# Kernel optimization log

Measured on AMD Instinct MI355X. Metric: run time of the kernel, lower is better.

Reference implementation:

```python
import jax, jax.numpy as jnp
import numpy as np

B, S, DIM = 2, 2048, 2048
NH, NKV = 16, 8
HD = DIM // NH  # 128
ROPE_THETA = 10000.0


def setup_inputs() -> dict:
    key = jax.random.key(0)
    ks = jax.random.split(key, 7)
    std = DIM ** -0.5
    x = jax.random.normal(ks[0], (B, S, DIM), jnp.float32)
    wq = jax.random.normal(ks[1], (NH * HD, DIM), jnp.float32) * std
    wk = jax.random.normal(ks[2], (NKV * HD, DIM), jnp.float32) * std
    wv = jax.random.normal(ks[3], (NKV * HD, DIM), jnp.float32) * std
    wo = jax.random.normal(ks[4], (DIM, NH * HD), jnp.float32) * std
    inv_freq = 1.0 / (ROPE_THETA ** (jnp.arange(0, HD, 2, dtype=jnp.float32) / HD))
    ang = jnp.arange(S, dtype=jnp.float32)[:, None] * inv_freq[None, :]  # [S, HD//2]
    freqs_cos = jnp.cos(ang)
    freqs_sin = jnp.sin(ang)
    # diffusion-style random per-batch token mask: t ~ U[0,1) per batch row
    t = jax.random.uniform(ks[5], (B, 1))
    mask = jax.random.uniform(ks[6], (B, S)) < t  # True = masked key
    mask = mask.at[:, 0].set(False)  # first token never masked
    return dict(x=x, wq=wq, wk=wk, wv=wv, wo=wo,
                freqs_cos=freqs_cos, freqs_sin=freqs_sin, mask=mask)


def _rope(x, cos, sin):
    # x: [b, s, h, d]; pairs (x[2i], x[2i+1]) rotated by angle[s, i]
    xr, xi = x[..., 0::2], x[..., 1::2]
    c = cos[None, :, None, :]
    s = sin[None, :, None, :]
    out = jnp.stack([xr * c - xi * s, xr * s + xi * c], axis=-1)
    return out.reshape(x.shape)


def reference(x, wq, wk, wv, wo, freqs_cos, freqs_sin, mask):
    b, s, _ = x.shape
    xq = jnp.einsum('bsd,ed->bse', x, wq).reshape(b, s, NH, HD)
    xk = jnp.einsum('bsd,ed->bse', x, wk).reshape(b, s, NKV, HD)
    xv = jnp.einsum('bsd,ed->bse', x, wv).reshape(b, s, NKV, HD)
    xq = _rope(xq, freqs_cos, freqs_sin)
    xk = _rope(xk, freqs_cos, freqs_sin)
    n_rep = NH // NKV
    xk = jnp.repeat(xk, n_rep, axis=2)  # repeat_kv (GQA)
    xv = jnp.repeat(xv, n_rep, axis=2)
    q = xq.transpose(0, 2, 1, 3)  # [b, h, s, d]
    k = xk.transpose(0, 2, 1, 3)
    v = xv.transpose(0, 2, 1, 3)
    scale = 1.0 / np.sqrt(HD).astype(np.float32)
    scores = jnp.einsum('bhqd,bhkd->bhqk', q, k) * scale  # [b, h, s, s]
    scores = jnp.where(mask[:, None, None, :], -jnp.inf, scores)
    probs = jax.nn.softmax(scores, axis=-1)
    out = jnp.einsum('bhqk,bhkd->bhqd', probs, v)
    out = out.transpose(0, 2, 1, 3).reshape(b, s, NH * HD)
    return jnp.einsum('bse,de->bsd', out, wo)
```

## Files before the change

kernel.cpp:

```cpp
#include <hip/hip_runtime.h>
#include <hip/hip_bf16.h>
#include <cstdint>
#include <cstddef>

#define S_LEN   2048
#define NHQ     16
#define NKV_H   8
#define HD_DIM  128
#define DMODEL  2048
#define BATCH   2
#define KVD     (NKV_H * HD_DIM)

typedef float f32x4  __attribute__((ext_vector_type(4)));
typedef __bf16 bf16x8 __attribute__((ext_vector_type(8)));

__device__ __forceinline__ void gload_lds16(const __bf16* g, __bf16* l) {
    __builtin_amdgcn_global_load_lds(
        (const __attribute__((address_space(1))) void*)g,
        (__attribute__((address_space(3))) void*)l, 16, 0, 0);
}

__global__ void sniff_x_kernel(const unsigned* __restrict__ x,
                               int* __restrict__ flag) {
    __shared__ int cnt;
    if (threadIdx.x == 0) cnt = 0;
    __syncthreads();
    int c = 0;
    for (int j = threadIdx.x; j < 1024; j += 256) {
        unsigned hw = x[j] & 0xFFFFu;
        unsigned e  = (hw >> 7) & 0xFF;
        if (hw == 0u || (e >= 118 && e <= 132)) c++;
    }
    atomicAdd(&cnt, c);
    __syncthreads();
    if (threadIdx.x == 0) *flag = (cnt > 512) ? 1 : 0;
}

__global__ void sniff_fc_kernel(const unsigned* __restrict__ fc,
                                int* __restrict__ flag) {
    if (threadIdx.x == 0) *flag = (fc[0] == 0x3F803F80u) ? 1 : 0;
}

__global__ void mask_norm_kernel(const unsigned char* __restrict__ mraw,
                                 unsigned char* __restrict__ mout, int n) {
    __shared__ int f_bf16, f_f32, f_u8;
    if (threadIdx.x == 0) { f_bf16 = 0; f_f32 = 0; f_u8 = 0; }
    __syncthreads();
    const unsigned* dw = (const unsigned*)mraw;
    int ndw = n / 4;
    for (int j = threadIdx.x; j < ndw; j += blockDim.x) {
        unsigned v = dw[j];
        if (v == 0x00003F80u || v == 0x3F803F80u) f_bf16 = 1;
        else if (v == 0x3F800000u) f_f32 = 1;
        else if (v & 0xFFFFFFFEu) f_u8 = 1;
    }
    __syncthreads();
    int layout;
    if (f_bf16) layout = 3;
    else if (f_f32) layout = 2;
    else if (f_u8) layout = 0;
    else layout = 1;
    for (int i = threadIdx.x; i < n; i += blockDim.x) {
        unsigned v;
        if (layout == 0)      v = mraw[i];
        else if (layout == 3) v = ((const unsigned short*)mraw)[i];
        else                  v = ((const unsigned*)mraw)[i];
        mout[i] = v ? 1u : 0u;
    }
}

__global__ __launch_bounds__(256)
void conv_bf16_kernel(const void* __restrict__ src, __bf16* __restrict__ dst,
                      int n8, const int* __restrict__ dflag) {
    int i = blockIdx.x * blockDim.x + threadIdx.x;
    if (i >= n8) return;
    size_t off = (size_t)i * 8;
    if (*dflag) {
        *reinterpret_cast<uint4*>(dst + off) =
            *reinterpret_cast<const uint4*>((const __bf16*)src + off);
    } else {
        const float* f = (const float*)src + off;
        float4 a = *reinterpret_cast<const float4*>(f);
        float4 b = *reinterpret_cast<const float4*>(f + 4);
        bf16x8 v;
        v[0] = (__bf16)a.x; v[1] = (__bf16)a.y; v[2] = (__bf16)a.z; v[3] = (__bf16)a.w;
        v[4] = (__bf16)b.x; v[5] = (__bf16)b.y; v[6] = (__bf16)b.z; v[7] = (__bf16)b.w;
        *reinterpret_cast<bf16x8*>(dst + off) = v;
    }
}

template <bool OUT_BF16>
__global__ __launch_bounds__(256)
void gemm_bt_async(const __bf16* __restrict__ A, const __bf16* __restrict__ Bw,
                   void* __restrict__ Cv, int M, int N, int K) {
    __shared__ __align__(16) __bf16 As[128 * 64];
    __shared__ __align__(16) __bf16 Bs[128 * 64];

    const int t    = threadIdx.x;
    const int w    = t >> 6;
    const int lane = t & 63;
    const int quad = lane >> 4;
    const int l16  = lane & 15;
    const int wm   = (w >> 1) * 64;
    const int wn   = (w & 1) * 64;
    const int m0   = blockIdx.x * 128;
    const int n0   = blockIdx.y * 128;
    const int rl   = lane >> 3;
    const int gl   = lane & 7;
    const int swA  = (quad) ;

    f32x4 acc[4][4];
#pragma unroll
    for (int i = 0; i < 4; ++i)
#pragma unroll
        for (int j = 0; j < 4; ++j) acc[i][j] = (f32x4){0.f, 0.f, 0.f, 0.f};

    for (int k0 = 0; k0 < K; k0 += 64) {
        __syncthreads();
#pragma unroll
        for (int p = 0; p < 4; ++p) {
            const int rowb = w * 32 + p * 8;
            const int r    = rowb + rl;
            const int gA   = gl ^ rl;
            gload_lds16(A  + (size_t)(m0 + r) * K + k0 + gA * 8, &As[rowb * 64]);
            gload_lds16(Bw + (size_t)(n0 + r) * K + k0 + gA * 8, &Bs[rowb * 64]);
        }
        __syncthreads();
#pragma unroll
        for (int ks = 0; ks < 2; ++ks) {
            const int G = ks * 4 + quad;
            const int gsw = (G ^ (l16 & 7)) * 8;
            bf16x8 af[4], bf[4];
#pragma unroll
            for (int i = 0; i < 4; ++i)
                af[i] = *reinterpret_cast<const bf16x8*>(
                    &As[(wm + i * 16 + l16) * 64 + gsw]);
#pragma unroll
            for (int j = 0; j < 4; ++j)
                bf[j] = *reinterpret_cast<const bf16x8*>(
                    &Bs[(wn + j * 16 + l16) * 64 + gsw]);
#pragma unroll
            for (int i = 0; i < 4; ++i)
#pragma unroll
                for (int j = 0; j < 4; ++j)
                    acc[i][j] = __builtin_amdgcn_mfma_f32_16x16x32_bf16(
                        af[i], bf[j], acc[i][j], 0, 0, 0);
        }
    }
    (void)swA;
#pragma unroll
    for (int i = 0; i < 4; ++i)
#pragma unroll
        for (int r = 0; r < 4; ++r) {
            size_t m = (size_t)(m0 + wm + i * 16 + quad * 4 + r);
#pragma unroll
            for (int j = 0; j < 4; ++j) {
                int n = n0 + wn + j * 16 + l16;
                if constexpr (OUT_BF16)
                    ((__hip_bfloat16*)Cv)[m * N + n] = __float2bfloat16(acc[i][j][r]);
                else
                    ((float*)Cv)[m * N + n] = acc[i][j][r];
            }
        }
}

__global__ void rope_kernel(__hip_bfloat16* __restrict__ xqk,
                            const void* __restrict__ cosv,
                            const void* __restrict__ sinv,
                            const int* __restrict__ dflag_fc,
                            int nheads, int npairs) {
    int idx = blockIdx.x * blockDim.x + threadIdx.x;
    if (idx >= npairs) return;
    int i  = idx & 63;
    int h  = (idx >> 6) % nheads;
    int bs = idx / (64 * nheads);
    int s  = bs & (S_LEN - 1);
    float c, sn;
    if (*dflag_fc) {
        c  = __bfloat162float(((const __hip_bfloat16*)cosv)[s * 64 + i]);
        sn = __bfloat162float(((const __hip_bfloat16*)sinv)[s * 64 + i]);
    } else {
        c  = ((const float*)cosv)[s * 64 + i];
        sn = ((const float*)sinv)[s * 64 + i];
    }
    unsigned* p = (unsigned*)(xqk + (size_t)bs * (nheads * HD_DIM) + h * HD_DIM) + i;
    unsigned u = *p;
    float xr = __uint_as_float(u << 16);
    float xi = __uint_as_float(u & 0xFFFF0000u);
    float o0 = xr * c - xi * sn;
    float o1 = xr * sn + xi * c;
    union { __hip_bfloat16 h2[2]; unsigned u32; } out;
    out.h2[0] = __float2bfloat16(o0);
    out.h2[1] = __float2bfloat16(o1);
    *p = out.u32;
}

__global__ __launch_bounds__(256)
void transpose_v_kernel(const __hip_bfloat16* __restrict__ xv,
                        __hip_bfloat16* __restrict__ vt) {
    __shared__ unsigned short T[32][36];
    const int t  = threadIdx.x;
    const int s0 = blockIdx.x * 32;
    const int d0 = blockIdx.y * 32;
    const int z  = blockIdx.z;
    const int b  = z >> 3;
    const int kv = z & 7;
    {
        int sr = t >> 3, dc = (t & 7) * 4;
        const unsigned short* p = (const unsigned short*)xv
            + (size_t)(b * S_LEN + s0 + sr) * KVD + kv * 128 + d0 + dc;
        uint2 v = *reinterpret_cast<const uint2*>(p);
        T[sr][dc + 0] = (unsigned short)(v.x & 0xFFFFu);
        T[sr][dc + 1] = (unsigned short)(v.x >> 16);
        T[sr][dc + 2] = (unsigned short)(v.y & 0xFFFFu);
        T[sr][dc + 3] = (unsigned short)(v.y >> 16);
    }
    __syncthreads();
    {
        int dr = t >> 3, sc = (t & 7) * 4;
        unsigned w0 = (unsigned)T[sc + 0][dr] | ((unsigned)T[sc + 1][dr] << 16);
        unsigned w1 = (unsigned)T[sc + 2][dr] | ((unsigned)T[sc + 3][dr] << 16);
        unsigned short* q = (unsigned short*)vt
            + ((size_t)z * 128 + d0 + dr) * S_LEN + s0 + sc;
        uint2 v; v.x = w0; v.y = w1;
        *reinterpret_cast<uint2*>(q) = v;
    }
}

__global__ __launch_bounds__(256)
void attn_mfma_kernel(const __hip_bfloat16* xq,
                      const __hip_bfloat16* __restrict__ xk,
                      const __hip_bfloat16* __restrict__ vt_g,
                      const unsigned char* __restrict__ msk,
                      __hip_bfloat16* att) {
    __shared__ __bf16 Qs[64][136];
    __shared__ __bf16 Ks[64][136];
    __shared__ __bf16 Vt[128][72];
    __shared__ __bf16 Ps[4][16][72];

    const int t    = threadIdx.x;
    const int w    = t >> 6;
    const int lane = t & 63;
    const int quad = lane >> 4;
    const int l16  = lane & 15;

    const int bid = blockIdx.x;
    const int qt  = bid & 31;
    const int h   = (bid >> 5) & (NHQ - 1);
    const int b   = bid >> 9;
    const int kvh = h >> 1;
    const int q0  = qt * 64;

#pragma unroll
    for (int i = 0; i < 4; ++i) {
        int p = t + i * 256;
        int r = p >> 4, c = p & 15;
        *reinterpret_cast<uint4*>(&Qs[r][c * 8]) =
            *reinterpret_cast<const uint4*>((const unsigned short*)xq
                + (size_t)(b * S_LEN + q0 + r) * DMODEL + h * 128 + c * 8);
    }

    float m_r[4], l_r[4];
    f32x4 o[8];
#pragma unroll
    for (int r = 0; r < 4; ++r) { m_r[r] = -INFINITY; l_r[r] = 0.f; }
#pragma unroll
    for (int d0 = 0; d0 < 8; ++d0) o[d0] = (f32x4){0.f, 0.f, 0.f, 0.f};

    const float scale = 0.08838834764831845f;

    for (int k0 = 0; k0 < S_LEN; k0 += 64) {
        __syncthreads();
#pragma unroll
        for (int i = 0; i < 4; ++i) {
            int p = t + i * 256;
            int r = p >> 4, c = p & 15;
            *reinterpret_cast<uint4*>(&Ks[r][c * 8]) =
                *reinterpret_cast<const uint4*>((const unsigned short*)xk
                    + (size_t)(b * S_LEN + k0 + r) * KVD + kvh * 128 + c * 8);
        }
#pragma unroll
        for (int i = 0; i < 4; ++i) {
            int p = t + i * 256;
            int d = p >> 3, c = p & 7;
            *reinterpret_cast<uint4*>(&Vt[d][c * 8]) =
                *reinterpret_cast<const uint4*>((const unsigned short*)vt_g
                    + ((size_t)(b * NKV_H + kvh) * 128 + d) * S_LEN + k0 + c * 8);
        }
        int mk[4];
#pragma unroll
        for (int n0 = 0; n0 < 4; ++n0)
            mk[n0] = msk[b * S_LEN + k0 + n0 * 16 + l16];
        __syncthreads();

        f32x4 sc4[4];
#pragma unroll
        for (int n0 = 0; n0 < 4; ++n0) sc4[n0] = (f32x4){0.f, 0.f, 0.f, 0.f};
#pragma unroll
        for (int ks = 0; ks < 4; ++ks) {
            int khd = ks * 32 + quad * 8;
            bf16x8 af = *reinterpret_cast<const bf16x8*>(&Qs[w * 16 + l16][khd]);
#pragma unroll
            for (int n0 = 0; n0 < 4; ++n0) {
                bf16x8 bf = *reinterpret_cast<const bf16x8*>(&Ks[n0 * 16 + l16][khd]);
                sc4[n0] = __builtin_amdgcn_mfma_f32_16x16x32_bf16(af, bf, sc4[n0], 0, 0, 0);
            }
        }

#pragma unroll
        for (int n0 = 0; n0 < 4; ++n0)
#pragma unroll
            for (int r = 0; r < 4; ++r) {
                float v = sc4[n0][r] * scale;
                sc4[n0][r] = mk[n0] ? -INFINITY : v;
            }
        float alpha[4];
#pragma unroll
        for (int r = 0; r < 4; ++r) {
            float rmax = fmaxf(fmaxf(sc4[0][r], sc4[1][r]), fmaxf(sc4[2][r], sc4[3][r]));
#pragma unroll
            for (int m = 1; m < 16; m <<= 1)
                rmax = fmaxf(rmax, __shfl_xor(rmax, m, 64));
            float mn = fmaxf(m_r[r], rmax);
            alpha[r] = __expf(m_r[r] - mn);
            m_r[r] = mn;
            float rs = 0.f;
#pragma unroll
            for (int n0 = 0; n0 < 4; ++n0) {
                float p = __expf(sc4[n0][r] - mn);
                sc4[n0][r] = p;
                rs += p;
            }
#pragma unroll
            for (int m = 1; m < 16; m <<= 1)
                rs += __shfl_xor(rs, m, 64);
            l_r[r] = l_r[r] * alpha[r] + rs;
        }
#pragma unroll
        for (int d0 = 0; d0 < 8; ++d0)
#pragma unroll
            for (int r = 0; r < 4; ++r) o[d0][r] *= alpha[r];

#pragma unroll
        for (int n0 = 0; n0 < 4; ++n0)
#pragma unroll
            for (int r = 0; r < 4; ++r)
                Ps[w][quad * 4 + r][n0 * 16 + l16] = (__bf16)sc4[n0][r];

#pragma unroll
        for (int kk = 0; kk < 64; kk += 32) {
            bf16x8 af = *reinterpret_cast<const bf16x8*>(&Ps[w][l16][kk + quad * 8]);
#pragma unroll
            for (int d0 = 0; d0 < 8; ++d0) {
                bf16x8 bf = *reinterpret_cast<const bf16x8*>(&Vt[d0 * 16 + l16][kk + quad * 8]);
                o[d0] = __builtin_amdgcn_mfma_f32_16x16x32_bf16(af, bf, o[d0], 0, 0, 0);
            }
        }
    }

    float inv[4];
#pragma unroll
    for (int r = 0; r < 4; ++r) inv[r] = 1.f / l_r[r];
#pragma unroll
    for (int d0 = 0; d0 < 8; ++d0)
#pragma unroll
        for (int r = 0; r < 4; ++r) {
            size_t row = (size_t)(b * S_LEN + q0 + w * 16 + quad * 4 + r);
            att[row * DMODEL + h * 128 + d0 * 16 + l16] =
                __float2bfloat16(o[d0][r] * inv[r]);
        }
}

extern "C" void kernel_launch(void* const* d_in, const int* in_sizes, int n_in,
                              void* d_out, int out_size, void* d_ws, size_t ws_size,
                              hipStream_t stream) {
    const void* x  = d_in[0];
    const void* wq = d_in[1];
    const void* wk = d_in[2];
    const void* wv = d_in[3];
    const void* wo = d_in[4];
    const void* fc = d_in[5];
    const void* fs = d_in[6];
    const unsigned char* mraw = (const unsigned char*)d_in[7];

    const int M = BATCH * S_LEN;
    char* wsb = (char*)d_ws;
    int* dflag_x  = (int*)wsb;
    int* dflag_fc = (int*)(wsb + 64);
    unsigned char* mnorm = (unsigned char*)(wsb + 128);
    __hip_bfloat16* xq = (__hip_bfloat16*)(wsb + 8192);
    __hip_bfloat16* xk = xq + (size_t)M * DMODEL;
    __hip_bfloat16* xv = xk + (size_t)M * KVD;
    __hip_bfloat16* att = xq;
    __hip_bfloat16* wob = xk;

    char* dob = (char*)d_out;
    __bf16* xb  = (__bf16*)dob;
    __bf16* wqb = (__bf16*)(dob + (16u << 20));
    __bf16* wkb = (__bf16*)(dob + (24u << 20));
    __bf16* wvb = (__bf16*)(dob + (28u << 20));
    __hip_bfloat16* vt = (__hip_bfloat16*)d_out;

    hipLaunchKernelGGL(sniff_x_kernel, dim3(1), dim3(256), 0, stream,
                       (const unsigned*)x, dflag_x);
    hipLaunchKernelGGL(sniff_fc_kernel, dim3(1), dim3(64), 0, stream,
                       (const unsigned*)fc, dflag_fc);
    hipLaunchKernelGGL(mask_norm_kernel, dim3(1), dim3(256), 0, stream,
                       mraw, mnorm, BATCH * S_LEN);

    hipLaunchKernelGGL(conv_bf16_kernel, dim3((M * DMODEL / 8) / 256), dim3(256), 0, stream,
                       x, xb, M * DMODEL / 8, dflag_x);
    hipLaunchKernelGGL(conv_bf16_kernel, dim3((DMODEL * DMODEL / 8) / 256), dim3(256), 0, stream,
                       wq, wqb, DMODEL * DMODEL / 8, dflag_x);
    hipLaunchKernelGGL(conv_bf16_kernel, dim3((KVD * DMODEL / 8) / 256), dim3(256), 0, stream,
                       wk, wkb, KVD * DMODEL / 8, dflag_x);
    hipLaunchKernelGGL(conv_bf16_kernel, dim3((KVD * DMODEL / 8) / 256), dim3(256), 0, stream,
                       wv, wvb, KVD * DMODEL / 8, dflag_x);

    hipLaunchKernelGGL((gemm_bt_async<true>), dim3(M / 128, DMODEL / 128), dim3(256), 0, stream,
                       xb, wqb, (void*)xq, M, DMODEL, DMODEL);
    hipLaunchKernelGGL((gemm_bt_async<true>), dim3(M / 128, KVD / 128), dim3(256), 0, stream,
                       xb, wkb, (void*)xk, M, KVD, DMODEL);
    hipLaunchKernelGGL((gemm_bt_async<true>), dim3(M / 128, KVD / 128), dim3(256), 0, stream,
                       xb, wvb, (void*)xv, M, KVD, DMODEL);

    int npq = M * NHQ * (HD_DIM / 2);
    int npk = M * NKV_H * (HD_DIM / 2);
    hipLaunchKernelGGL(rope_kernel, dim3(npq / 256), dim3(256), 0, stream,
                       xq, fc, fs, dflag_fc, NHQ, npq);
    hipLaunchKernelGGL(rope_kernel, dim3(npk / 256), dim3(256), 0, stream,
                       xk, fc, fs, dflag_fc, NKV_H, npk);

    hipLaunchKernelGGL(transpose_v_kernel, dim3(S_LEN / 32, HD_DIM / 32, BATCH * NKV_H),
                       dim3(256), 0, stream, xv, vt);

    hipLaunchKernelGGL(attn_mfma_kernel, dim3(BATCH * NHQ * (S_LEN / 64)), dim3(256), 0, stream,
                       xq, xk, vt, mnorm, att);

    hipLaunchKernelGGL(conv_bf16_kernel, dim3((DMODEL * DMODEL / 8) / 256), dim3(256), 0, stream,
                       wo, (__bf16*)wob, DMODEL * DMODEL / 8, dflag_x);
    hipLaunchKernelGGL((gemm_bt_async<false>), dim3(M / 128, DMODEL / 128), dim3(256), 0, stream,
                       (const __bf16*)att, (const __bf16*)wob, d_out, M, DMODEL, DMODEL);
}
```

Measured before the change: 529.8 us.

## Rework attention kernel with register Q, async swizzled K/V LDS loads, exp2 softmax

The attention kernel now keeps each wave's Q fragments in registers instead of staging them in shared memory. K and V tiles are loaded with direct global-to-LDS async loads into XOR-swizzled unpadded layouts, and the P tile uses the same swizzle. The softmax folds log2(e) into the scale and uses exp2f. The aim is to cut LDS traffic, bank conflicts and register round-trips on the loads, at the cost of more index arithmetic and the correctness risk that comes with the swizzle.

```diff
diff --git a/kernel.cpp b/kernel.cpp
--- a/kernel.cpp
+++ b/kernel.cpp
@@ -107,7 +107,6 @@
     const int n0   = blockIdx.y * 128;
     const int rl   = lane >> 3;
     const int gl   = lane & 7;
-    const int swA  = (quad) ;
 
     f32x4 acc[4][4];
 #pragma unroll
@@ -147,7 +146,6 @@
                         af[i], bf[j], acc[i][j], 0, 0, 0);
         }
     }
-    (void)swA;
 #pragma unroll
     for (int i = 0; i < 4; ++i)
 #pragma unroll
@@ -228,15 +226,14 @@
 }
 
 __global__ __launch_bounds__(256)
-void attn_mfma_kernel(const __hip_bfloat16* xq,
-                      const __hip_bfloat16* __restrict__ xk,
-                      const __hip_bfloat16* __restrict__ vt_g,
-                      const unsigned char* __restrict__ msk,
-                      __hip_bfloat16* att) {
-    __shared__ __bf16 Qs[64][136];
-    __shared__ __bf16 Ks[64][136];
-    __shared__ __bf16 Vt[128][72];
-    __shared__ __bf16 Ps[4][16][72];
+void attn_mfma2_kernel(const __hip_bfloat16* xq,
+                       const __hip_bfloat16* __restrict__ xk,
+                       const __hip_bfloat16* __restrict__ vt_g,
+                       const unsigned char* __restrict__ msk,
+                       __hip_bfloat16* att) {
+    __shared__ __align__(16) __bf16 Ks[64 * 128];
+    __shared__ __align__(16) __bf16 Vt[128 * 64];
+    __shared__ __align__(16) __bf16 Ps[4][16][64];
 
     const int t    = threadIdx.x;
     const int w    = t >> 6;
@@ -251,13 +248,13 @@
     const int kvh = h >> 1;
     const int q0  = qt * 64;
 
-#pragma unroll
-    for (int i = 0; i < 4; ++i) {
-        int p = t + i * 256;
-        int r = p >> 4, c = p & 15;
-        *reinterpret_cast<uint4*>(&Qs[r][c * 8]) =
-            *reinterpret_cast<const uint4*>((const unsigned short*)xq
-                + (size_t)(b * S_LEN + q0 + r) * DMODEL + h * 128 + c * 8);
+    bf16x8 qf[4];
+    {
+        const __bf16* qrow = (const __bf16*)xq
+            + (size_t)(b * S_LEN + q0 + w * 16 + l16) * DMODEL + h * 128 + quad * 8;
+#pragma unroll
+        for (int ks = 0; ks < 4; ++ks)
+            qf[ks] = *reinterpret_cast<const bf16x8*>(qrow + ks * 32);
     }
 
     float m_r[4], l_r[4];
@@ -267,25 +264,29 @@
 #pragma unroll
     for (int d0 = 0; d0 < 8; ++d0) o[d0] = (f32x4){0.f, 0.f, 0.f, 0.f};
 
-    const float scale = 0.08838834764831845f;
+    const float scale2 = 0.08838834764831845f * 1.4426950408889634f;
+
+    const int krl = lane >> 4, kgl = lane & 15;
+    const int vrl = lane >> 3, vgl = lane & 7;
 
     for (int k0 = 0; k0 < S_LEN; k0 += 64) {
         __syncthreads();
 #pragma unroll
-        for (int i = 0; i < 4; ++i) {
-            int p = t + i * 256;
-            int r = p >> 4, c = p & 15;
-            *reinterpret_cast<uint4*>(&Ks[r][c * 8]) =
-                *reinterpret_cast<const uint4*>((const unsigned short*)xk
-                    + (size_t)(b * S_LEN + k0 + r) * KVD + kvh * 128 + c * 8);
-        }
-#pragma unroll
-        for (int i = 0; i < 4; ++i) {
-            int p = t + i * 256;
-            int d = p >> 3, c = p & 7;
-            *reinterpret_cast<uint4*>(&Vt[d][c * 8]) =
-                *reinterpret_cast<const uint4*>((const unsigned short*)vt_g
-                    + ((size_t)(b * NKV_H + kvh) * 128 + d) * S_LEN + k0 + c * 8);
+        for (int p = 0; p < 4; ++p) {
+            const int row  = w * 16 + p * 4 + krl;
+            const int srcg = kgl ^ (row & 7);
+            gload_lds16((const __bf16*)xk + (size_t)(b * S_LEN + k0 + row) * KVD
+                            + kvh * 128 + srcg * 8,
+                        &Ks[(w * 16 + p * 4) * 128]);
+        }
+#pragma unroll
+        for (int p = 0; p < 4; ++p) {
+            const int row  = w * 32 + p * 8 + vrl;
+            const int srcg = vgl ^ (row & 7);
+            gload_lds16((const __bf16*)vt_g
+                            + ((size_t)(b * NKV_H + kvh) * 128 + row) * S_LEN
+                            + k0 + srcg * 8,
+                        &Vt[(w * 32 + p * 8) * 64]);
         }
         int mk[4];
 #pragma unroll
@@ -298,12 +299,13 @@
         for (int n0 = 0; n0 < 4; ++n0) sc4[n0] = (f32x4){0.f, 0.f, 0.f, 0.f};
 #pragma unroll
         for (int ks = 0; ks < 4; ++ks) {
-            int khd = ks * 32 + quad * 8;
-            bf16x8 af = *reinterpret_cast<const bf16x8*>(&Qs[w * 16 + l16][khd]);
+            const int G = ks * 4 + quad;
 #pragma unroll
             for (int n0 = 0; n0 < 4; ++n0) {
-                bf16x8 bf = *reinterpret_cast<const bf16x8*>(&Ks[n0 * 16 + l16][khd]);
-                sc4[n0] = __builtin_amdgcn_mfma_f32_16x16x32_bf16(af, bf, sc4[n0], 0, 0, 0);
+                const int row  = n0 * 16 + l16;
+                const int slot = G ^ (row & 7);
+                bf16x8 bf = *reinterpret_cast<const bf16x8*>(&Ks[row * 128 + slot * 8]);
+                sc4[n0] = __builtin_amdgcn_mfma_f32_16x16x32_bf16(qf[ks], bf, sc4[n0], 0, 0, 0);
             }
         }
 
@@ -311,7 +313,7 @@
         for (int n0 = 0; n0 < 4; ++n0)
 #pragma unroll
             for (int r = 0; r < 4; ++r) {
-                float v = sc4[n0][r] * scale;
+                float v = sc4[n0][r] * scale2;
                 sc4[n0][r] = mk[n0] ? -INFINITY : v;
             }
         float alpha[4];
@@ -322,12 +324,12 @@
             for (int m = 1; m < 16; m <<= 1)
                 rmax = fmaxf(rmax, __shfl_xor(rmax, m, 64));
             float mn = fmaxf(m_r[r], rmax);
-            alpha[r] = __expf(m_r[r] - mn);
+            alpha[r] = exp2f(m_r[r] - mn);
             m_r[r] = mn;
             float rs = 0.f;
 #pragma unroll
             for (int n0 = 0; n0 < 4; ++n0) {
-                float p = __expf(sc4[n0][r] - mn);
+                float p = exp2f(sc4[n0][r] - mn);
                 sc4[n0][r] = p;
                 rs += p;
             }
@@ -342,17 +344,27 @@
             for (int r = 0; r < 4; ++r) o[d0][r] *= alpha[r];
 
 #pragma unroll
-        for (int n0 = 0; n0 < 4; ++n0)
-#pragma unroll
-            for (int r = 0; r < 4; ++r)
-                Ps[w][quad * 4 + r][n0 * 16 + l16] = (__bf16)sc4[n0][r];
+        for (int n0 = 0; n0 < 4; ++n0) {
+            const int G = n0 * 2 + (l16 >> 3);
+            const int cs = l16 & 7;
+#pragma unroll
+            for (int r = 0; r < 4; ++r) {
+                const int row  = quad * 4 + r;
+                const int slot = G ^ (row & 7);
+                Ps[w][row][slot * 8 + cs] = (__bf16)sc4[n0][r];
+            }
+        }
 
 #pragma unroll
         for (int kk = 0; kk < 64; kk += 32) {
-            bf16x8 af = *reinterpret_cast<const bf16x8*>(&Ps[w][l16][kk + quad * 8]);
+            const int Gp    = (kk >> 3) + quad;
+            const int slotp = Gp ^ (l16 & 7);
+            bf16x8 af = *reinterpret_cast<const bf16x8*>(&Ps[w][l16][slotp * 8]);
 #pragma unroll
             for (int d0 = 0; d0 < 8; ++d0) {
-                bf16x8 bf = *reinterpret_cast<const bf16x8*>(&Vt[d0 * 16 + l16][kk + quad * 8]);
+                const int row  = d0 * 16 + l16;
+                const int slot = Gp ^ (row & 7);
+                bf16x8 bf = *reinterpret_cast<const bf16x8*>(&Vt[row * 64 + slot * 8]);
                 o[d0] = __builtin_amdgcn_mfma_f32_16x16x32_bf16(af, bf, o[d0], 0, 0, 0);
             }
         }
@@ -434,7 +446,7 @@
     hipLaunchKernelGGL(transpose_v_kernel, dim3(S_LEN / 32, HD_DIM / 32, BATCH * NKV_H),
                        dim3(256), 0, stream, xv, vt);
 
-    hipLaunchKernelGGL(attn_mfma_kernel, dim3(BATCH * NHQ * (S_LEN / 64)), dim3(256), 0, stream,
+    hipLaunchKernelGGL(attn_mfma2_kernel, dim3(BATCH * NHQ * (S_LEN / 64)), dim3(256), 0, stream,
                        xq, xk, vt, mnorm, att);
 
     hipLaunchKernelGGL(conv_bf16_kernel, dim3((DMODEL * DMODEL / 8) / 256), dim3(256), 0, stream,
```

Result: no change. 521.2 us (-1.6%).
